# Kernel optimization log

Hardware: AMD Instinct MI355X
Metric: run time of the kernel (lower is better)

The kernel has to match this reference:

```python
import jax, jax.numpy as jnp
import numpy as np

NUM_CLASSES = 100
EPS = 1e-8  # torch F.cosine_similarity default eps


def setup_inputs() -> dict:
    key = jax.random.key(0)
    k1, k2 = jax.random.split(key)
    feat = jax.random.normal(k1, (100000, 512), dtype=jnp.float32)
    label = jax.random.randint(k2, (100000,), 0, NUM_CLASSES, dtype=jnp.int64)
    return {"feat": feat, "label": label}


def reference(feat, label):
    # Per-class mean (segment mean) -- replaces the Python loop over classes.
    sums = jax.ops.segment_sum(feat, label, num_segments=NUM_CLASSES)          # [C, D]
    counts = jax.ops.segment_sum(jnp.ones_like(label, dtype=feat.dtype), label,
                                 num_segments=NUM_CLASSES)                      # [C]
    means = sums / jnp.maximum(counts, 1.0)[:, None]                            # [C, D]

    # Only the gathered (own-class) column of the sim matrix is returned,
    # so compute cos(feat[i], means[label[i]]) directly.
    cent = means[label]                                                         # [N, D]
    dot = jnp.sum(feat * cent, axis=-1)                                         # [N]
    n_feat = jnp.maximum(jnp.linalg.norm(feat, axis=-1), EPS)
    n_cent = jnp.maximum(jnp.linalg.norm(cent, axis=-1), EPS)
    return dot / (n_feat * n_cent)
```

## Files before the change

kernel.cpp:

```cpp
#include <hip/hip_runtime.h>

#define NCLS 100
#define DIM  512
#define EPSV 1e-8f

#define DSPL 8
#define CH   192
#define NW   4
#define SCALE    262144.0f
#define INVSCALE (1.0f / 262144.0f)

__global__ __launch_bounds__(256) void sum_kernel(const float* __restrict__ feat,
                                                  const int* __restrict__ label,
                                                  int* __restrict__ partial,
                                                  int* __restrict__ cntp, int n) {
    __shared__ int acc[NCLS * 64];
    __shared__ int hcnt[NCLS];
    const int tid = threadIdx.x;
    const int ds  = blockIdx.x;
    const int ch  = blockIdx.y;

    for (int i = tid; i < NCLS * 64; i += 256) acc[i] = 0;
    if (ds == 0)
        for (int i = tid; i < NCLS; i += 256) hcnt[i] = 0;
    __syncthreads();

    const int rpc  = (n + CH - 1) / CH;
    const int r0   = ch * rpc;
    const int rows = max(0, min(rpc, n - r0));
    const int w    = tid >> 6;
    const int lane = tid & 63;
    const int lo   = (rows * w) / NW;
    const int hi   = (rows * (w + 1)) / NW;
    const float* fb = feat + ds * 64 + lane;

    int r = lo;
    for (; r + 8 <= hi; r += 8) {
        float v[8];
        #pragma unroll
        for (int k = 0; k < 8; ++k) v[k] = fb[(size_t)(r0 + r + k) * DIM];
        const int myl = label[r0 + r + (lane & 7)];
        int c[8];
        #pragma unroll
        for (int k = 0; k < 8; ++k) c[k] = __shfl(myl, k, 64);

        #pragma unroll
        for (int k = 0; k < 8; ++k)
            atomicAdd(&acc[c[k] * 64 + lane], __float2int_rn(v[k] * SCALE));
        if (ds == 0 && lane == 0) {
            #pragma unroll
            for (int k = 0; k < 8; ++k) atomicAdd(&hcnt[c[k]], 1);
        }
    }
    for (; r < hi; ++r) {
        const float v = fb[(size_t)(r0 + r) * DIM];
        const int   c = label[r0 + r];
        atomicAdd(&acc[c * 64 + lane], __float2int_rn(v * SCALE));
        if (ds == 0 && lane == 0) atomicAdd(&hcnt[c], 1);
    }
    __syncthreads();

    int4* d4 = (int4*)(partial + ((size_t)ch * DSPL + ds) * (NCLS * 64));
    const int4* s4 = (const int4*)acc;
    for (int i = tid; i < NCLS * 16; i += 256) d4[i] = s4[i];
    if (ds == 0)
        for (int i = tid; i < NCLS; i += 256) cntp[ch * 128 + i] = hcnt[i];
}

__global__ __launch_bounds__(512) void finalize_kernel(const int* __restrict__ partial,
                                                       const int* __restrict__ cntp,
                                                       float* __restrict__ mhat) {
    const int c = blockIdx.x;
    const int t = threadIdx.x;
    __shared__ int   csh[8];
    __shared__ float red[8];
    __shared__ float invsh;

    int pc = 0;
    for (int ch = t; ch < CH; ch += 512) pc += cntp[ch * 128 + c];
    #pragma unroll
    for (int o = 32; o; o >>= 1) pc += __shfl_down(pc, o, 64);
    if ((t & 63) == 0) csh[t >> 6] = pc;
    __syncthreads();
    if (t == 0) {
        int tot = 0;
        #pragma unroll
        for (int k = 0; k < 8; ++k) tot += csh[k];
        invsh = INVSCALE / fmaxf((float)tot, 1.0f);
    }
    __syncthreads();
    const float inv = invsh;

    const int ds  = t >> 6;
    const int off = t & 63;
    const int* p = partial + ((size_t)ds * NCLS + c) * 64 + off;
    const size_t stride = (size_t)DSPL * NCLS * 64;
    long long a0 = 0, a1 = 0, a2 = 0, a3 = 0;
    for (int ch = 0; ch < CH; ch += 4) {
        a0 += p[(size_t)(ch + 0) * stride];
        a1 += p[(size_t)(ch + 1) * stride];
        a2 += p[(size_t)(ch + 2) * stride];
        a3 += p[(size_t)(ch + 3) * stride];
    }
    const float m = (float)((a0 + a1) + (a2 + a3)) * inv;

    float ss = m * m;
    #pragma unroll
    for (int o = 32; o; o >>= 1) ss += __shfl_down(ss, o, 64);
    if ((t & 63) == 0) red[t >> 6] = ss;
    __syncthreads();
    float tot = 0.f;
    #pragma unroll
    for (int k = 0; k < 8; ++k) tot += red[k];
    const float q = 1.0f / fmaxf(sqrtf(tot), EPSV);
    mhat[(size_t)c * DIM + t] = m * q;
}

__global__ __launch_bounds__(256) void cos_kernel(const float* __restrict__ feat,
                                                  const int* __restrict__ label,
                                                  const float* __restrict__ mhat,
                                                  float* __restrict__ out, int n) {
    const int lane = threadIdx.x & 63;
    const int wv   = threadIdx.x >> 6;
    const int cl   = lane >> 4;
    const int t    = lane & 15;

    const int row = blockIdx.x * 16 + wv * 4 + cl;
    const bool ok = row < n;
    const int rr = ok ? row : (n - 1);

    const int c = label[rr];
    const float4* f4 = (const float4*)(feat + (size_t)rr * DIM);
    const float4* m4 = (const float4*)(mhat + (size_t)c  * DIM);

    float4 a[8], b[8];
    #pragma unroll
    for (int j = 0; j < 8; ++j) a[j] = f4[t + 16 * j];
    #pragma unroll
    for (int j = 0; j < 8; ++j) b[j] = m4[t + 16 * j];

    float dot = 0.0f, nf = 0.0f;
    #pragma unroll
    for (int j = 0; j < 8; ++j) {
        dot += a[j].x * b[j].x + a[j].y * b[j].y + a[j].z * b[j].z + a[j].w * b[j].w;
        nf  += a[j].x * a[j].x + a[j].y * a[j].y + a[j].z * a[j].z + a[j].w * a[j].w;
    }

    #pragma unroll
    for (int off = 8; off; off >>= 1) {
        dot += __shfl_xor(dot, off, 64);
        nf  += __shfl_xor(nf,  off, 64);
    }
    if (t == 0 && ok) {
        out[row] = dot / fmaxf(sqrtf(nf), EPSV);
    }
}

extern "C" void kernel_launch(void* const* d_in, const int* in_sizes, int n_in,
                              void* d_out, int out_size, void* d_ws, size_t ws_size,
                              hipStream_t stream) {
    const float* feat  = (const float*)d_in[0];
    const int*   label = (const int*)d_in[1];
    float*       out   = (float*)d_out;
    const int n = in_sizes[0] / DIM;

    float* mhat    = (float*)d_ws;
    int*   cntp    = (int*)(mhat + NCLS * DIM);
    int*   partial = cntp + CH * 128;

    dim3 sg(DSPL, CH);
    sum_kernel<<<sg, 256, 0, stream>>>(feat, label, partial, cntp, n);

    finalize_kernel<<<NCLS, 512, 0, stream>>>(partial, cntp, mhat);

    cos_kernel<<<(n + 15) / 16, 256, 0, stream>>>(feat, label, mhat, out, n);
}
```

Measured before the change: 332.2 us.

## Reduce class sums via global atomics and drop count normalization

The sum kernel now accumulates each block's shared-memory fixed-point sums directly into a single global class-sum buffer with atomics. This replaces writing large per-chunk partials that a finalize kernel then had to re-read. Per-class counts are removed because dividing the mean by a positive count does not change its unit direction, so the cosine is unchanged. Each block handles 128 columns with a larger row batch, and an extra memset is added to clear the accumulator.

```diff
diff --git a/kernel.cpp b/kernel.cpp
--- a/kernel.cpp
+++ b/kernel.cpp
@@ -4,116 +4,82 @@
 #define DIM  512
 #define EPSV 1e-8f
 
-#define DSPL 8
-#define CH   192
-#define NW   4
-#define SCALE    262144.0f
-#define INVSCALE (1.0f / 262144.0f)
+#define DSPL  4
+#define CH    192
+#define BATCH 16
+#define SCALE 262144.0f
 
-__global__ __launch_bounds__(256) void sum_kernel(const float* __restrict__ feat,
-                                                  const int* __restrict__ label,
-                                                  int* __restrict__ partial,
-                                                  int* __restrict__ cntp, int n) {
-    __shared__ int acc[NCLS * 64];
-    __shared__ int hcnt[NCLS];
+__global__ __launch_bounds__(256, 4) void sum_kernel(const float* __restrict__ feat,
+                                                     const int* __restrict__ label,
+                                                     int* __restrict__ S, int n) {
+    __shared__ int acc[NCLS * 128];
     const int tid = threadIdx.x;
     const int ds  = blockIdx.x;
     const int ch  = blockIdx.y;
 
-    for (int i = tid; i < NCLS * 64; i += 256) acc[i] = 0;
-    if (ds == 0)
-        for (int i = tid; i < NCLS; i += 256) hcnt[i] = 0;
+    for (int i = tid; i < NCLS * 128; i += 256) acc[i] = 0;
     __syncthreads();
 
     const int rpc  = (n + CH - 1) / CH;
+    const int rows = min(rpc, n - ch * rpc);
     const int r0   = ch * rpc;
-    const int rows = max(0, min(rpc, n - r0));
     const int w    = tid >> 6;
     const int lane = tid & 63;
-    const int lo   = (rows * w) / NW;
-    const int hi   = (rows * (w + 1)) / NW;
-    const float* fb = feat + ds * 64 + lane;
+    const int lo   = (rows * w) >> 2;
+    const int hi   = (rows * (w + 1)) >> 2;
+    const float* f0 = feat + (size_t)ds * 128 + lane;
 
     int r = lo;
-    for (; r + 8 <= hi; r += 8) {
-        float v[8];
+    for (; r + BATCH <= hi; r += BATCH) {
+        float va[BATCH], vb[BATCH];
         #pragma unroll
-        for (int k = 0; k < 8; ++k) v[k] = fb[(size_t)(r0 + r + k) * DIM];
-        const int myl = label[r0 + r + (lane & 7)];
-        int c[8];
+        for (int k = 0; k < BATCH; ++k) {
+            const float* p = f0 + (size_t)(r0 + r + k) * DIM;
+            va[k] = p[0];
+            vb[k] = p[64];
+        }
+        const int myl = label[r0 + r + (lane & (BATCH - 1))];
         #pragma unroll
-        for (int k = 0; k < 8; ++k) c[k] = __shfl(myl, k, 64);
-
-        #pragma unroll
-        for (int k = 0; k < 8; ++k)
-            atomicAdd(&acc[c[k] * 64 + lane], __float2int_rn(v[k] * SCALE));
-        if (ds == 0 && lane == 0) {
-            #pragma unroll
-            for (int k = 0; k < 8; ++k) atomicAdd(&hcnt[c[k]], 1);
+        for (int k = 0; k < BATCH; ++k) {
+            const int c = __shfl(myl, k, 64);
+            int* a = &acc[c * 128 + lane];
+            atomicAdd(a,      __float2int_rn(va[k] * SCALE));
+            atomicAdd(a + 64, __float2int_rn(vb[k] * SCALE));
         }
     }
     for (; r < hi; ++r) {
-        const float v = fb[(size_t)(r0 + r) * DIM];
-        const int   c = label[r0 + r];
-        atomicAdd(&acc[c * 64 + lane], __float2int_rn(v * SCALE));
-        if (ds == 0 && lane == 0) atomicAdd(&hcnt[c], 1);
+        const int c = label[r0 + r];
+        const float* p = f0 + (size_t)(r0 + r) * DIM;
+        int* a = &acc[c * 128 + lane];
+        atomicAdd(a,      __float2int_rn(p[0]  * SCALE));
+        atomicAdd(a + 64, __float2int_rn(p[64] * SCALE));
     }
     __syncthreads();
 
-    int4* d4 = (int4*)(partial + ((size_t)ch * DSPL + ds) * (NCLS * 64));
-    const int4* s4 = (const int4*)acc;
-    for (int i = tid; i < NCLS * 16; i += 256) d4[i] = s4[i];
-    if (ds == 0)
-        for (int i = tid; i < NCLS; i += 256) cntp[ch * 128 + i] = hcnt[i];
+    for (int i = tid; i < NCLS * 128; i += 256) {
+        const int c = i >> 7;
+        const int j = i & 127;
+        atomicAdd(&S[(size_t)c * DIM + ds * 128 + j], acc[i]);
+    }
 }
 
-__global__ __launch_bounds__(512) void finalize_kernel(const int* __restrict__ partial,
-                                                       const int* __restrict__ cntp,
-                                                       float* __restrict__ mhat) {
+__global__ __launch_bounds__(512) void norm_kernel(const int* __restrict__ S,
+                                                   float* __restrict__ mhat) {
     const int c = blockIdx.x;
     const int t = threadIdx.x;
-    __shared__ int   csh[8];
-    __shared__ float red[8];
-    __shared__ float invsh;
+    const float v = (float)S[(size_t)c * DIM + t];
 
-    int pc = 0;
-    for (int ch = t; ch < CH; ch += 512) pc += cntp[ch * 128 + c];
-    #pragma unroll
-    for (int o = 32; o; o >>= 1) pc += __shfl_down(pc, o, 64);
-    if ((t & 63) == 0) csh[t >> 6] = pc;
-    __syncthreads();
-    if (t == 0) {
-        int tot = 0;
-        #pragma unroll
-        for (int k = 0; k < 8; ++k) tot += csh[k];
-        invsh = INVSCALE / fmaxf((float)tot, 1.0f);
-    }
-    __syncthreads();
-    const float inv = invsh;
-
-    const int ds  = t >> 6;
-    const int off = t & 63;
-    const int* p = partial + ((size_t)ds * NCLS + c) * 64 + off;
-    const size_t stride = (size_t)DSPL * NCLS * 64;
-    long long a0 = 0, a1 = 0, a2 = 0, a3 = 0;
-    for (int ch = 0; ch < CH; ch += 4) {
-        a0 += p[(size_t)(ch + 0) * stride];
-        a1 += p[(size_t)(ch + 1) * stride];
-        a2 += p[(size_t)(ch + 2) * stride];
-        a3 += p[(size_t)(ch + 3) * stride];
-    }
-    const float m = (float)((a0 + a1) + (a2 + a3)) * inv;
-
-    float ss = m * m;
+    float ss = v * v;
     #pragma unroll
     for (int o = 32; o; o >>= 1) ss += __shfl_down(ss, o, 64);
+    __shared__ float red[8];
     if ((t & 63) == 0) red[t >> 6] = ss;
     __syncthreads();
     float tot = 0.f;
     #pragma unroll
     for (int k = 0; k < 8; ++k) tot += red[k];
-    const float q = 1.0f / fmaxf(sqrtf(tot), EPSV);
-    mhat[(size_t)c * DIM + t] = m * q;
+    const float q = (tot > 0.f) ? (1.0f / sqrtf(tot)) : 0.0f;
+    mhat[(size_t)c * DIM + t] = v * q;
 }
 
 __global__ __launch_bounds__(256) void cos_kernel(const float* __restrict__ feat,
@@ -164,14 +130,13 @@
     float*       out   = (float*)d_out;
     const int n = in_sizes[0] / DIM;
 
-    float* mhat    = (float*)d_ws;
-    int*   cntp    = (int*)(mhat + NCLS * DIM);
-    int*   partial = cntp + CH * 128;
+    int*   S    = (int*)d_ws;
+    float* mhat = (float*)(S + NCLS * DIM);
+
+    hipMemsetAsync(S, 0, NCLS * DIM * sizeof(int), stream);
 
     dim3 sg(DSPL, CH);
-    sum_kernel<<<sg, 256, 0, stream>>>(feat, label, partial, cntp, n);
-
-    finalize_kernel<<<NCLS, 512, 0, stream>>>(partial, cntp, mhat);
-
+    sum_kernel<<<sg, 256, 0, stream>>>(feat, label, S, n);
+    norm_kernel<<<NCLS, 512, 0, stream>>>(S, mhat);
     cos_kernel<<<(n + 15) / 16, 256, 0, stream>>>(feat, label, mhat, out, n);
 }
```

Measured after the change: 335.5 us. Within noise of the previous version (+1.0%).
